# Optimization experiments

Measured on AMD Instinct MI355X. Metric: run time of the kernel, lower is better.

The kernel has to match this reference:

```python
import jax, jax.numpy as jnp
import numpy as np

N = 200000   # active voxels
K = 27       # 3^3 kernel offsets
C = 64       # feature channels (in == out -> residual is Identity)
EPS = 1e-5   # BatchNorm eps (torch default)


def setup_inputs() -> dict:
    key = jax.random.key(0)
    k0, k1, k2, k3 = jax.random.split(key, 4)
    x = jax.random.normal(k0, (N, C), dtype=jnp.float32)
    # neighbor map: for each output voxel and kernel offset, index of input voxel
    nbr_idx = jax.random.randint(k1, (N, K), 0, N, dtype=jnp.int64)
    W1 = jax.random.normal(k2, (K, C, C), dtype=jnp.float32) * 0.05
    W2 = jax.random.normal(k3, (K, C, C), dtype=jnp.float32) * 0.05
    gamma1 = jnp.ones((C,), jnp.float32)
    beta1 = jnp.zeros((C,), jnp.float32)
    gamma2 = jnp.ones((C,), jnp.float32)
    beta2 = jnp.zeros((C,), jnp.float32)
    return {"x": x, "nbr_idx": nbr_idx, "W1": W1, "gamma1": gamma1,
            "beta1": beta1, "W2": W2, "gamma2": gamma2, "beta2": beta2}


def batchnorm(x, gamma, beta):
    # train-mode BatchNorm1d over the voxel axis (biased variance)
    mu = x.mean(axis=0)
    var = x.var(axis=0)
    return (x - mu) * jax.lax.rsqrt(var + EPS) * gamma + beta


def sparse_conv(x, nbr_idx, W):
    # gather-GEMM-scatter sparse conv, streamed over the 27 kernel offsets
    # x: [N, Cin], nbr_idx: [N, K], W: [K, Cin, Cout]
    def body(acc, kw):
        idx, Wk = kw                      # idx: [N], Wk: [Cin, Cout]
        return acc + x[idx] @ Wk, None
    acc0 = jnp.zeros((x.shape[0], W.shape[2]), x.dtype)
    acc, _ = jax.lax.scan(body, acc0, (nbr_idx.T, W))
    return acc


def reference(x, nbr_idx, W1, gamma1, beta1, W2, gamma2, beta2):
    residual = x  # in_features == out_features -> Identity residual
    out = sparse_conv(jax.nn.relu(batchnorm(x, gamma1, beta1)), nbr_idx, W1)
    out = sparse_conv(jax.nn.relu(batchnorm(out, gamma2, beta2)), nbr_idx, W2)
    return out + residual
```

## Files before the change

kernel.cpp:

```cpp
#include <hip/hip_runtime.h>


#define KOFF 27

typedef __bf16 bf16x8 __attribute__((ext_vector_type(8)));
typedef float floatx4 __attribute__((ext_vector_type(4)));

__device__ __forceinline__ unsigned short f2bf(float x) {
    union { float f; unsigned int u; } v; v.f = x;
    unsigned int u = v.u;
    unsigned int r = u + 0x7FFFu + ((u >> 16) & 1u);
    return (unsigned short)(r >> 16);
}
__device__ __forceinline__ float bf2f(unsigned short s) {
    union { float f; unsigned int u; } v; v.u = ((unsigned int)s) << 16; return v.f;
}

__global__ void prep2(const float* __restrict__ W1, const float* __restrict__ W2,
                      unsigned short* __restrict__ W1f, unsigned short* __restrict__ W2f,
                      const float* __restrict__ x, float* __restrict__ stats,
                      int total) {
    int b = blockIdx.x, t = threadIdx.x;
    if (b < 54) {
        __shared__ float sW[64 * 68];
        int k = b % 27;
        const float* src = (b < 27 ? W1 : W2) + k * 4096;
        unsigned short* dst = (b < 27 ? W1f : W2f) + (size_t)k * 4096;
        #pragma unroll
        for (int i = 0; i < 4; ++i) {
            int i4 = t + i * 256;
            float4 v = ((const float4*)src)[i4];
            int f = i4 * 4, r = f >> 6, c = f & 63;
            sW[r * 68 + c]     = v.x;
            sW[r * 68 + c + 1] = v.y;
            sW[r * 68 + c + 2] = v.z;
            sW[r * 68 + c + 3] = v.w;
        }
        __syncthreads();
        int fi = (t >> 5) & 7, ct = fi >> 1, ks = fi & 1;
        unsigned short o[16];
        #pragma unroll
        for (int d = 0; d < 2; ++d) {
            int lane2 = (t * 2 + d) & 63, q = lane2 >> 4, l15 = lane2 & 15;
            #pragma unroll
            for (int j = 0; j < 8; ++j) {
                int cin = ks * 32 + q * 8 + j, cout = ct * 16 + l15;
                o[d * 8 + j] = f2bf(sW[cin * 68 + cout]);
            }
        }
        ((uint4*)(dst + t * 16))[0] = *(const uint4*)(o);
        ((uint4*)(dst + t * 16))[1] = *(const uint4*)(o + 8);
        return;
    }
    __shared__ float s[128];
    if (t < 128) s[t] = 0.f;
    __syncthreads();
    int i = (b - 54) * 256 + t;
    int stride = (gridDim.x - 54) * 256;
    int c = i & 63;
    float s1 = 0.f, s2 = 0.f;
    for (; i < total; i += stride) { float v = x[i]; s1 += v; s2 += v * v; }
    atomicAdd(&s[c], s1);
    atomicAdd(&s[64 + c], s2);
    __syncthreads();
    if (t < 64) { atomicAdd(&stats[t], s[t]); atomicAdd(&stats[64 + t], s[64 + t]); }
}

__global__ void bn_relu_f32(const float* __restrict__ in, const float* __restrict__ sums,
                            const float* __restrict__ gamma, const float* __restrict__ beta,
                            unsigned short* __restrict__ out, int total4, float invN) {
    __shared__ float sab[128];
    int t = threadIdx.x;
    if (t < 64) {
        float mu  = sums[t] * invN;
        float var = fmaxf(sums[64 + t] * invN - mu * mu, 0.f);
        float a   = gamma[t] * rsqrtf(var + 1e-5f);
        sab[t] = a; sab[64 + t] = beta[t] - mu * a;
    }
    __syncthreads();
    int i = blockIdx.x * blockDim.x + t;
    int stride = gridDim.x * blockDim.x;
    for (; i < total4; i += stride) {
        float4 v = ((const float4*)in)[i];
        int c0 = (i << 2) & 63;
        ushort4 o;
        o.x = f2bf(fmaxf(sab[c0]     * v.x + sab[64 + c0],     0.f));
        o.y = f2bf(fmaxf(sab[c0 + 1] * v.y + sab[64 + c0 + 1], 0.f));
        o.z = f2bf(fmaxf(sab[c0 + 2] * v.z + sab[64 + c0 + 2], 0.f));
        o.w = f2bf(fmaxf(sab[c0 + 3] * v.w + sab[64 + c0 + 3], 0.f));
        ((ushort4*)out)[i] = o;
    }
}

__global__ void bn_relu_b16(const unsigned short* __restrict__ in, const float* __restrict__ sums,
                            const float* __restrict__ gamma, const float* __restrict__ beta,
                            unsigned short* __restrict__ out, int total8, float invN) {
    __shared__ float sab[128];
    int t = threadIdx.x;
    if (t < 64) {
        float mu  = sums[t] * invN;
        float var = fmaxf(sums[64 + t] * invN - mu * mu, 0.f);
        float a   = gamma[t] * rsqrtf(var + 1e-5f);
        sab[t] = a; sab[64 + t] = beta[t] - mu * a;
    }
    __syncthreads();
    int i = blockIdx.x * blockDim.x + t;
    int stride = gridDim.x * blockDim.x;
    for (; i < total8; i += stride) {
        uint4 v = ((const uint4*)in)[i];
        int c0 = (i << 3) & 63;
        unsigned int w[4] = {v.x, v.y, v.z, v.w};
        unsigned int o[4];
        #pragma unroll
        for (int p = 0; p < 4; ++p) {
            float f0 = bf2f((unsigned short)(w[p] & 0xffff));
            float f1 = bf2f((unsigned short)(w[p] >> 16));
            int c = c0 + p * 2;
            unsigned short r0 = f2bf(fmaxf(sab[c]     * f0 + sab[64 + c],     0.f));
            unsigned short r1 = f2bf(fmaxf(sab[c + 1] * f1 + sab[64 + c + 1], 0.f));
            o[p] = (unsigned int)r0 | ((unsigned int)r1 << 16);
        }
        ((uint4*)out)[i] = make_uint4(o[0], o[1], o[2], o[3]);
    }
}

#define MFMA(a, b, c) __builtin_amdgcn_mfma_f32_16x16x32_bf16(a, b, c, 0, 0, 0)
#define WAIT_LGKM0() __builtin_amdgcn_s_waitcnt(0xC07F)

__global__ __launch_bounds__(256, 4) void spconv(
        const unsigned short* __restrict__ h,
        const int* __restrict__ idx,
        const unsigned short* __restrict__ Wf,
        unsigned short* __restrict__ outb,
        float* __restrict__ outf,
        const float* __restrict__ resid,
        float* __restrict__ stats,
        int N) {
    __shared__ float4 arena[1088];
    __shared__ float sred[128];
    unsigned short* sBb = (unsigned short*)arena;
    float* sE = (float*)arena;

    int t = threadIdx.x, lane = t & 63, wid = t >> 6;
    int q = lane >> 4, l15 = lane & 15;
    int base = blockIdx.x * 128;
    if (t < 128) sred[t] = 0.f;

    int r0 = base + wid * 32 + l15;
    int r1 = r0 + 16;
    const int* ip0 = idx + (size_t)min(r0, N - 1) * KOFF;
    const int* ip1 = idx + (size_t)min(r1, N - 1) * KOFF;
    int qo = q * 8;

    floatx4 acc[2][4];
    #pragma unroll
    for (int a_ = 0; a_ < 2; ++a_)
        #pragma unroll
        for (int b_ = 0; b_ < 4; ++b_)
            acc[a_][b_] = floatx4{0.f, 0.f, 0.f, 0.f};

    bf16x8 A0[4], A1[4], A2[4];
    {
        int g0 = ip0[0], g1 = ip1[0];
        const unsigned short* p0 = h + ((size_t)g0 << 6) + qo;
        const unsigned short* p1 = h + ((size_t)g1 << 6) + qo;
        A0[0] = *(const bf16x8*)p0; A0[1] = *(const bf16x8*)(p0 + 32);
        A0[2] = *(const bf16x8*)p1; A0[3] = *(const bf16x8*)(p1 + 32);
        g0 = ip0[1]; g1 = ip1[1];
        p0 = h + ((size_t)g0 << 6) + qo;
        p1 = h + ((size_t)g1 << 6) + qo;
        A1[0] = *(const bf16x8*)p0; A1[1] = *(const bf16x8*)(p0 + 32);
        A1[2] = *(const bf16x8*)p1; A1[3] = *(const bf16x8*)(p1 + 32);
    }
    int gc0 = ip0[2], gc1 = ip1[2];

    const uint4* Wf4 = (const uint4*)Wf;
    int so = wid * 64 + lane;
    uint4 bs0 = Wf4[so], bs1 = Wf4[256 + so];
    ((uint4*)sBb)[so] = bs0; ((uint4*)sBb)[256 + so] = bs1;
    bs0 = Wf4[512 + so]; bs1 = Wf4[512 + 256 + so];

#define COMPUTE(ACUR, CB) {                                                    \
    const bf16x8* bp = (const bf16x8*)(sBb + (CB) * 4096);                     \
    bf16x8 f0 = bp[lane], f1 = bp[64 + lane], f2 = bp[128 + lane], f3 = bp[192 + lane]; \
    acc[0][0] = MFMA(ACUR[0], f0, acc[0][0]); acc[0][0] = MFMA(ACUR[1], f1, acc[0][0]); \
    acc[0][1] = MFMA(ACUR[0], f2, acc[0][1]); acc[0][1] = MFMA(ACUR[1], f3, acc[0][1]); \
    acc[1][0] = MFMA(ACUR[2], f0, acc[1][0]); acc[1][0] = MFMA(ACUR[3], f1, acc[1][0]); \
    acc[1][1] = MFMA(ACUR[2], f2, acc[1][1]); acc[1][1] = MFMA(ACUR[3], f3, acc[1][1]); \
    f0 = bp[256 + lane]; f1 = bp[320 + lane]; f2 = bp[384 + lane]; f3 = bp[448 + lane]; \
    acc[0][2] = MFMA(ACUR[0], f0, acc[0][2]); acc[0][2] = MFMA(ACUR[1], f1, acc[0][2]); \
    acc[0][3] = MFMA(ACUR[0], f2, acc[0][3]); acc[0][3] = MFMA(ACUR[1], f3, acc[0][3]); \
    acc[1][2] = MFMA(ACUR[2], f0, acc[1][2]); acc[1][2] = MFMA(ACUR[3], f1, acc[1][2]); \
    acc[1][3] = MFMA(ACUR[2], f2, acc[1][3]); acc[1][3] = MFMA(ACUR[3], f3, acc[1][3]); \
}

#define BODY_FULL(ACUR, ALD, KRT, CB, NB) {                                    \
    WAIT_LGKM0();                                                              \
    __builtin_amdgcn_s_barrier();                                              \
    ((uint4*)sBb)[(NB) * 512 + so] = bs0;                                      \
    ((uint4*)sBb)[(NB) * 512 + 256 + so] = bs1;                                \
    bs0 = Wf4[((KRT) + 2) * 512 + so]; bs1 = Wf4[((KRT) + 2) * 512 + 256 + so];\
    {                                                                          \
        const unsigned short* p0 = h + ((size_t)gc0 << 6) + qo;                \
        const unsigned short* p1 = h + ((size_t)gc1 << 6) + qo;                \
        ALD[0] = *(const bf16x8*)p0; ALD[1] = *(const bf16x8*)(p0 + 32);       \
        ALD[2] = *(const bf16x8*)p1; ALD[3] = *(const bf16x8*)(p1 + 32);       \
    }                                                                          \
    gc0 = ip0[(KRT) + 3]; gc1 = ip1[(KRT) + 3];                                \
    COMPUTE(ACUR, CB)                                                          \
}

    #pragma unroll 1
    for (int kk = 0; kk < 24; kk += 6) {
        BODY_FULL(A0, A2, kk + 0, 0, 1)
        BODY_FULL(A1, A0, kk + 1, 1, 0)
        BODY_FULL(A2, A1, kk + 2, 0, 1)
        BODY_FULL(A0, A2, kk + 3, 1, 0)
        BODY_FULL(A1, A0, kk + 4, 0, 1)
        BODY_FULL(A2, A1, kk + 5, 1, 0)
    }
    {
        WAIT_LGKM0();
        __builtin_amdgcn_s_barrier();
        ((uint4*)sBb)[512 + so] = bs0; ((uint4*)sBb)[512 + 256 + so] = bs1;
        bs0 = Wf4[26 * 512 + so]; bs1 = Wf4[26 * 512 + 256 + so];
        {
            const unsigned short* p0 = h + ((size_t)gc0 << 6) + qo;
            const unsigned short* p1 = h + ((size_t)gc1 << 6) + qo;
            A2[0] = *(const bf16x8*)p0; A2[1] = *(const bf16x8*)(p0 + 32);
            A2[2] = *(const bf16x8*)p1; A2[3] = *(const bf16x8*)(p1 + 32);
        }
        COMPUTE(A0, 0)
    }
    {
        WAIT_LGKM0();
        __builtin_amdgcn_s_barrier();
        ((uint4*)sBb)[so] = bs0; ((uint4*)sBb)[256 + so] = bs1;
        COMPUTE(A1, 1)
    }
    {
        WAIT_LGKM0();
        __builtin_amdgcn_s_barrier();
        COMPUTE(A2, 0)
    }
#undef BODY_FULL
#undef COMPUTE

    if (stats) {
        #pragma unroll
        for (int ct = 0; ct < 4; ++ct) {
            float s1 = 0.f, s2 = 0.f;
            #pragma unroll
            for (int rt = 0; rt < 2; ++rt)
                #pragma unroll
                for (int r = 0; r < 4; ++r) {
                    int rowc = base + wid * 32 + rt * 16 + q * 4 + r;
                    float vv = (rowc < N) ? acc[rt][ct][r] : 0.f;
                    s1 += vv; s2 += vv * vv;
                }
            s1 += __shfl_xor(s1, 16); s2 += __shfl_xor(s2, 16);
            s1 += __shfl_xor(s1, 32); s2 += __shfl_xor(s2, 32);
            if (q == 0) {
                atomicAdd(&sred[ct * 16 + l15], s1);
                atomicAdd(&sred[64 + ct * 16 + l15], s2);
            }
        }
    }

    __syncthreads();

    #pragma unroll
    for (int hf = 0; hf < 2; ++hf) {
        if ((wid >> 1) == hf) {
            int lrow0 = (wid & 1) * 32;
            #pragma unroll
            for (int rt = 0; rt < 2; ++rt)
                #pragma unroll
                for (int ct = 0; ct < 4; ++ct)
                    #pragma unroll
                    for (int r = 0; r < 4; ++r)
                        sE[(lrow0 + rt * 16 + q * 4 + r) * 68 + ct * 16 + l15] = acc[rt][ct][r];
        }
        __syncthreads();
        if (hf == 0 && stats && t < 64) {
            atomicAdd(&stats[t], sred[t]);
            atomicAdd(&stats[64 + t], sred[64 + t]);
        }
        int rr = t >> 2, cc = t & 3;
        int grow = base + hf * 64 + rr;
        if (grow < N) {
            const float* sp = sE + rr * 68 + cc * 16;
            if (outb) {
                unsigned short o[16];
                #pragma unroll
                for (int j = 0; j < 16; ++j) o[j] = f2bf(sp[j]);
                unsigned short* op = outb + ((size_t)grow << 6) + cc * 16;
                ((uint4*)op)[0] = *(const uint4*)(o);
                ((uint4*)op)[1] = *(const uint4*)(o + 8);
            } else {
                const float* rp = resid + ((size_t)grow << 6) + cc * 16;
                float* op = outf + ((size_t)grow << 6) + cc * 16;
                #pragma unroll
                for (int j = 0; j < 4; ++j) {
                    float4 v = *(const float4*)(sp + j * 4);
                    float4 rv = *(const float4*)(rp + j * 4);
                    v.x += rv.x; v.y += rv.y; v.z += rv.z; v.w += rv.w;
                    *(float4*)(op + j * 4) = v;
                }
            }
        }
        if (hf == 0) __syncthreads();
    }
}

extern "C" void kernel_launch(void* const* d_in, const int* in_sizes, int n_in,
                              void* d_out, int out_size, void* d_ws, size_t ws_size,
                              hipStream_t stream) {
    const float* x      = (const float*)d_in[0];
    const int*   nbr    = (const int*)  d_in[1];
    const float* W1     = (const float*)d_in[2];
    const float* gamma1 = (const float*)d_in[3];
    const float* beta1  = (const float*)d_in[4];
    const float* W2     = (const float*)d_in[5];
    const float* gamma2 = (const float*)d_in[6];
    const float* beta2  = (const float*)d_in[7];
    float* out = (float*)d_out;

    int N = in_sizes[0] / 64;
    float invN = 1.0f / (float)N;

    char* ws = (char*)d_ws;
    float*          stats = (float*)ws;
    unsigned short* W1f   = (unsigned short*)(ws + 4096);
    unsigned short* W2f   = W1f + 110592;
    unsigned short* hbuf  = W2f + 110592;
    unsigned short* out1b = hbuf + (size_t)N * 64;

    int nb = (N + 127) / 128;

    hipMemsetAsync(stats, 0, 2048, stream);
    prep2<<<54 + 512, 256, 0, stream>>>(W1, W2, W1f, W2f, x, stats, N * 64);
    bn_relu_f32<<<768, 256, 0, stream>>>(x, stats, gamma1, beta1, hbuf, N * 16, invN);
    spconv<<<nb, 256, 0, stream>>>(hbuf, nbr, W1f, out1b, nullptr, nullptr, stats + 256, N);
    bn_relu_b16<<<768, 256, 0, stream>>>(out1b, stats + 256, gamma2, beta2, hbuf, N * 8, invN);
    spconv<<<nb, 256, 0, stream>>>(hbuf, nbr, W2f, nullptr, out, x, nullptr, N);
}
```

Baseline: 427.1 us.

## Stream weights via global_load_lds triple buffer and vectorize BN stats reduction

The spconv weight staging moves from register-staged global loads plus LDS stores to direct global-to-LDS DMA loads with a three-slot LDS ring. Synchronisation now uses explicit vmcnt waits, inline-asm ds_read_b128 and scheduling barriers, with a three-deep gather prefetch of the neighbour rows. This is meant to free the VGPRs that held staged weights and to overlap weight streaming with the MFMA work. It also vectorizes the first BN stats reduction in prep2 to float4 loads. In exchange LDS use grows to 24KB per block, which may limit occupancy, and the hand-tuned vmcnt counts are fragile.

Result: no change. 428.9 us (+0.4%).

```diff
diff --git a/kernel.cpp b/kernel.cpp
--- a/kernel.cpp
+++ b/kernel.cpp
@@ -19,7 +19,7 @@
 __global__ void prep2(const float* __restrict__ W1, const float* __restrict__ W2,
                       unsigned short* __restrict__ W1f, unsigned short* __restrict__ W2f,
                       const float* __restrict__ x, float* __restrict__ stats,
-                      int total) {
+                      int total4) {
     int b = blockIdx.x, t = threadIdx.x;
     if (b < 54) {
         __shared__ float sW[64 * 68];
@@ -57,11 +57,20 @@
     __syncthreads();
     int i = (b - 54) * 256 + t;
     int stride = (gridDim.x - 54) * 256;
-    int c = i & 63;
-    float s1 = 0.f, s2 = 0.f;
-    for (; i < total; i += stride) { float v = x[i]; s1 += v; s2 += v * v; }
-    atomicAdd(&s[c], s1);
-    atomicAdd(&s[64 + c], s2);
+    float a0 = 0.f, a1 = 0.f, a2 = 0.f, a3 = 0.f;
+    float b0 = 0.f, b1 = 0.f, b2 = 0.f, b3 = 0.f;
+    for (; i < total4; i += stride) {
+        float4 v = ((const float4*)x)[i];
+        a0 += v.x; b0 += v.x * v.x;
+        a1 += v.y; b1 += v.y * v.y;
+        a2 += v.z; b2 += v.z * v.z;
+        a3 += v.w; b3 += v.w * v.w;
+    }
+    int c0 = (t << 2) & 63;
+    atomicAdd(&s[c0],     a0); atomicAdd(&s[c0 + 1],     a1);
+    atomicAdd(&s[c0 + 2], a2); atomicAdd(&s[c0 + 3],     a3);
+    atomicAdd(&s[64 + c0],     b0); atomicAdd(&s[64 + c0 + 1], b1);
+    atomicAdd(&s[64 + c0 + 2], b2); atomicAdd(&s[64 + c0 + 3], b3);
     __syncthreads();
     if (t < 64) { atomicAdd(&stats[t], s[t]); atomicAdd(&stats[64 + t], s[64 + t]); }
 }
@@ -125,7 +134,12 @@
 }
 
 #define MFMA(a, b, c) __builtin_amdgcn_mfma_f32_16x16x32_bf16(a, b, c, 0, 0, 0)
-#define WAIT_LGKM0() __builtin_amdgcn_s_waitcnt(0xC07F)
+
+#define FENCE() { asm volatile("" ::: "memory"); __builtin_amdgcn_sched_barrier(0); }
+
+#define GLDS(GP, LOFS) __builtin_amdgcn_global_load_lds( \
+    (const __attribute__((address_space(1))) unsigned int*)(GP), \
+    (__attribute__((address_space(3))) unsigned int*)(ar + (LOFS)), 16, 0, 0)
 
 __global__ __launch_bounds__(256, 4) void spconv(
         const unsigned short* __restrict__ h,
@@ -136,9 +150,9 @@
         const float* __restrict__ resid,
         float* __restrict__ stats,
         int N) {
-    __shared__ float4 arena[1088];
+    __shared__ float4 arena[1536];
     __shared__ float sred[128];
-    unsigned short* sBb = (unsigned short*)arena;
+    char* ar = (char*)arena;
     float* sE = (float*)arena;
 
     int t = threadIdx.x, lane = t & 63, wid = t >> 6;
@@ -152,6 +166,11 @@
     const int* ip1 = idx + (size_t)min(r1, N - 1) * KOFF;
     int qo = q * 8;
 
+    const char* gw = (const char*)Wf + (size_t)(wid * 1024 + lane * 16);
+    int ldss = wid * 1024;
+    unsigned av0 = (unsigned)(size_t)((__attribute__((address_space(3))) char*)ar)
+                 + (unsigned)(lane * 16);
+
     floatx4 acc[2][4];
     #pragma unroll
     for (int a_ = 0; a_ < 2; ++a_)
@@ -159,92 +178,107 @@
         for (int b_ = 0; b_ < 4; ++b_)
             acc[a_][b_] = floatx4{0.f, 0.f, 0.f, 0.f};
 
+#define GATHER(DST, G0, G1) { \
+    const unsigned short* p0_ = h + ((size_t)(G0) << 6) + qo; \
+    const unsigned short* p1_ = h + ((size_t)(G1) << 6) + qo; \
+    DST[0] = *(const bf16x8*)p0_; DST[1] = *(const bf16x8*)(p0_ + 32); \
+    DST[2] = *(const bf16x8*)p1_; DST[3] = *(const bf16x8*)(p1_ + 32); \
+}
+
     bf16x8 A0[4], A1[4], A2[4];
-    {
-        int g0 = ip0[0], g1 = ip1[0];
-        const unsigned short* p0 = h + ((size_t)g0 << 6) + qo;
-        const unsigned short* p1 = h + ((size_t)g1 << 6) + qo;
-        A0[0] = *(const bf16x8*)p0; A0[1] = *(const bf16x8*)(p0 + 32);
-        A0[2] = *(const bf16x8*)p1; A0[3] = *(const bf16x8*)(p1 + 32);
-        g0 = ip0[1]; g1 = ip1[1];
-        p0 = h + ((size_t)g0 << 6) + qo;
-        p1 = h + ((size_t)g1 << 6) + qo;
-        A1[0] = *(const bf16x8*)p0; A1[1] = *(const bf16x8*)(p0 + 32);
-        A1[2] = *(const bf16x8*)p1; A1[3] = *(const bf16x8*)(p1 + 32);
-    }
-    int gc0 = ip0[2], gc1 = ip1[2];
-
-    const uint4* Wf4 = (const uint4*)Wf;
-    int so = wid * 64 + lane;
-    uint4 bs0 = Wf4[so], bs1 = Wf4[256 + so];
-    ((uint4*)sBb)[so] = bs0; ((uint4*)sBb)[256 + so] = bs1;
-    bs0 = Wf4[512 + so]; bs1 = Wf4[512 + 256 + so];
-
-#define COMPUTE(ACUR, CB) {                                                    \
-    const bf16x8* bp = (const bf16x8*)(sBb + (CB) * 4096);                     \
-    bf16x8 f0 = bp[lane], f1 = bp[64 + lane], f2 = bp[128 + lane], f3 = bp[192 + lane]; \
+    GLDS(gw,         ldss);
+    GLDS(gw + 4096,  ldss + 4096);
+    GLDS(gw + 8192,  8192 + ldss);
+    GLDS(gw + 12288, 8192 + ldss + 4096);
+    FENCE();
+    { int g0 = ip0[0], g1 = ip1[0]; GATHER(A0, g0, g1); }
+    { int g0 = ip0[1], g1 = ip1[1]; GATHER(A1, g0, g1); }
+    { int g0 = ip0[2], g1 = ip1[2]; GATHER(A2, g0, g1); }
+    int gc0 = ip0[3], gc1 = ip1[3];
+    FENCE();
+
+#define COMPUTE(ACUR, AV) { \
+    unsigned av_ = (AV); \
+    bf16x8 f0, f1, f2, f3; \
+    asm volatile("ds_read_b128 %0, %1 offset:0"    : "=v"(f0) : "v"(av_)); \
+    asm volatile("ds_read_b128 %0, %1 offset:1024" : "=v"(f1) : "v"(av_)); \
+    asm volatile("ds_read_b128 %0, %1 offset:2048" : "=v"(f2) : "v"(av_)); \
+    asm volatile("ds_read_b128 %0, %1 offset:3072" : "=v"(f3) : "v"(av_)); \
+    asm volatile("s_waitcnt lgkmcnt(0)" ::: "memory"); \
+    __builtin_amdgcn_sched_barrier(0); \
     acc[0][0] = MFMA(ACUR[0], f0, acc[0][0]); acc[0][0] = MFMA(ACUR[1], f1, acc[0][0]); \
     acc[0][1] = MFMA(ACUR[0], f2, acc[0][1]); acc[0][1] = MFMA(ACUR[1], f3, acc[0][1]); \
     acc[1][0] = MFMA(ACUR[2], f0, acc[1][0]); acc[1][0] = MFMA(ACUR[3], f1, acc[1][0]); \
     acc[1][1] = MFMA(ACUR[2], f2, acc[1][1]); acc[1][1] = MFMA(ACUR[3], f3, acc[1][1]); \
-    f0 = bp[256 + lane]; f1 = bp[320 + lane]; f2 = bp[384 + lane]; f3 = bp[448 + lane]; \
+    FENCE(); \
+    asm volatile("ds_read_b128 %0, %1 offset:4096" : "=v"(f0) : "v"(av_)); \
+    asm volatile("ds_read_b128 %0, %1 offset:5120" : "=v"(f1) : "v"(av_)); \
+    asm volatile("ds_read_b128 %0, %1 offset:6144" : "=v"(f2) : "v"(av_)); \
+    asm volatile("ds_read_b128 %0, %1 offset:7168" : "=v"(f3) : "v"(av_)); \
+    asm volatile("s_waitcnt lgkmcnt(0)" ::: "memory"); \
+    __builtin_amdgcn_sched_barrier(0); \
     acc[0][2] = MFMA(ACUR[0], f0, acc[0][2]); acc[0][2] = MFMA(ACUR[1], f1, acc[0][2]); \
     acc[0][3] = MFMA(ACUR[0], f2, acc[0][3]); acc[0][3] = MFMA(ACUR[1], f3, acc[0][3]); \
     acc[1][2] = MFMA(ACUR[2], f0, acc[1][2]); acc[1][2] = MFMA(ACUR[3], f1, acc[1][2]); \
     acc[1][3] = MFMA(ACUR[2], f2, acc[1][3]); acc[1][3] = MFMA(ACUR[3], f3, acc[1][3]); \
 }
 
-#define BODY_FULL(ACUR, ALD, KRT, CB, NB) {                                    \
-    WAIT_LGKM0();                                                              \
-    __builtin_amdgcn_s_barrier();                                              \
-    ((uint4*)sBb)[(NB) * 512 + so] = bs0;                                      \
-    ((uint4*)sBb)[(NB) * 512 + 256 + so] = bs1;                                \
-    bs0 = Wf4[((KRT) + 2) * 512 + so]; bs1 = Wf4[((KRT) + 2) * 512 + 256 + so];\
-    {                                                                          \
-        const unsigned short* p0 = h + ((size_t)gc0 << 6) + qo;                \
-        const unsigned short* p1 = h + ((size_t)gc1 << 6) + qo;                \
-        ALD[0] = *(const bf16x8*)p0; ALD[1] = *(const bf16x8*)(p0 + 32);       \
-        ALD[2] = *(const bf16x8*)p1; ALD[3] = *(const bf16x8*)(p1 + 32);       \
-    }                                                                          \
-    gc0 = ip0[(KRT) + 3]; gc1 = ip1[(KRT) + 3];                                \
-    COMPUTE(ACUR, CB)                                                          \
-}
+#define STEP_WAIT(VM) \
+    asm volatile("s_waitcnt vmcnt(" VM ")" ::: "memory"); \
+    __builtin_amdgcn_sched_barrier(0); \
+    __builtin_amdgcn_s_barrier(); \
+    FENCE();
+
+#define STAGE(K, WOFS) \
+    GLDS(gw + (size_t)((K) + 2) * 8192,        (WOFS) + ldss); \
+    GLDS(gw + (size_t)((K) + 2) * 8192 + 4096, (WOFS) + ldss + 4096); \
+    FENCE();
+
+#define BODY_FULL(K, VM, AB, RD, WOFS) { \
+    STEP_WAIT(VM) \
+    STAGE(K, WOFS) \
+    COMPUTE(AB, av0 + (RD)); \
+    FENCE(); \
+    GATHER(AB, gc0, gc1); \
+    gc0 = ip0[(K) + 4]; gc1 = ip1[(K) + 4]; \
+    FENCE(); \
+}
+
+    BODY_FULL(0, "2",  A0, 0,     16384)
+    BODY_FULL(1, "14", A1, 8192,  0)
 
     #pragma unroll 1
-    for (int kk = 0; kk < 24; kk += 6) {
-        BODY_FULL(A0, A2, kk + 0, 0, 1)
-        BODY_FULL(A1, A0, kk + 1, 1, 0)
-        BODY_FULL(A2, A1, kk + 2, 0, 1)
-        BODY_FULL(A0, A2, kk + 3, 1, 0)
-        BODY_FULL(A1, A0, kk + 4, 0, 1)
-        BODY_FULL(A2, A1, kk + 5, 1, 0)
+    for (int k = 2; k < 23; k += 3) {
+        BODY_FULL(k,     "14", A2, 16384, 8192)
+        BODY_FULL(k + 1, "14", A0, 0,     16384)
+        BODY_FULL(k + 2, "14", A1, 8192,  0)
     }
     {
-        WAIT_LGKM0();
-        __builtin_amdgcn_s_barrier();
-        ((uint4*)sBb)[512 + so] = bs0; ((uint4*)sBb)[512 + 256 + so] = bs1;
-        bs0 = Wf4[26 * 512 + so]; bs1 = Wf4[26 * 512 + 256 + so];
-        {
-            const unsigned short* p0 = h + ((size_t)gc0 << 6) + qo;
-            const unsigned short* p1 = h + ((size_t)gc1 << 6) + qo;
-            A2[0] = *(const bf16x8*)p0; A2[1] = *(const bf16x8*)(p0 + 32);
-            A2[2] = *(const bf16x8*)p1; A2[3] = *(const bf16x8*)(p1 + 32);
-        }
-        COMPUTE(A0, 0)
+        STEP_WAIT("14")
+        STAGE(23, 8192)
+        COMPUTE(A2, av0 + 16384);
+        FENCE();
+        GATHER(A2, gc0, gc1);
+        FENCE();
     }
     {
-        WAIT_LGKM0();
-        __builtin_amdgcn_s_barrier();
-        ((uint4*)sBb)[so] = bs0; ((uint4*)sBb)[256 + so] = bs1;
-        COMPUTE(A1, 1)
+        STEP_WAIT("12")
+        STAGE(24, 16384)
+        COMPUTE(A0, av0 + 0);
     }
     {
-        WAIT_LGKM0();
-        __builtin_amdgcn_s_barrier();
-        COMPUTE(A2, 0)
+        STEP_WAIT("6")
+        COMPUTE(A1, av0 + 8192);
+    }
+    {
+        STEP_WAIT("0")
+        COMPUTE(A2, av0 + 16384);
     }
 #undef BODY_FULL
+#undef STAGE
+#undef STEP_WAIT
 #undef COMPUTE
+#undef GATHER
 
     if (stats) {
         #pragma unroll
@@ -339,7 +373,7 @@
     int nb = (N + 127) / 128;
 
     hipMemsetAsync(stats, 0, 2048, stream);
-    prep2<<<54 + 512, 256, 0, stream>>>(W1, W2, W1f, W2f, x, stats, N * 64);
+    prep2<<<54 + 512, 256, 0, stream>>>(W1, W2, W1f, W2f, x, stats, N * 16);
     bn_relu_f32<<<768, 256, 0, stream>>>(x, stats, gamma1, beta1, hbuf, N * 16, invN);
     spconv<<<nb, 256, 0, stream>>>(hbuf, nbr, W1f, out1b, nullptr, nullptr, stats + 256, N);
     bn_relu_b16<<<768, 256, 0, stream>>>(out1b, stats + 256, gamma2, beta2, hbuf, N * 8, invN);
```

## Fuse second BN+ReLU into conv gather and vectorize input stats reduction

Applied to the files above, without the earlier changes.

Removes the standalone bf16 BatchNorm+ReLU kernel. The second sparse conv now applies the per-channel affine and ReLU to gathered rows in registers before the MFMAs. This saves one full read-write pass over the intermediate activations and a kernel launch. In exchange, every gathered row (27x per voxel) is normalized again, which adds VALU work and registers inside the MFMA loop. The stats reduction in prep2 also now reads float4 with four per-channel accumulators.

After: 448.3 us. 1.05x slower.

```diff
diff --git a/kernel.cpp b/kernel.cpp
--- a/kernel.cpp
+++ b/kernel.cpp
@@ -19,7 +19,7 @@
 __global__ void prep2(const float* __restrict__ W1, const float* __restrict__ W2,
                       unsigned short* __restrict__ W1f, unsigned short* __restrict__ W2f,
                       const float* __restrict__ x, float* __restrict__ stats,
-                      int total) {
+                      int total4) {
     int b = blockIdx.x, t = threadIdx.x;
     if (b < 54) {
         __shared__ float sW[64 * 68];
@@ -57,11 +57,20 @@
     __syncthreads();
     int i = (b - 54) * 256 + t;
     int stride = (gridDim.x - 54) * 256;
-    int c = i & 63;
-    float s1 = 0.f, s2 = 0.f;
-    for (; i < total; i += stride) { float v = x[i]; s1 += v; s2 += v * v; }
-    atomicAdd(&s[c], s1);
-    atomicAdd(&s[64 + c], s2);
+    float a0 = 0.f, a1 = 0.f, a2 = 0.f, a3 = 0.f;
+    float b0 = 0.f, b1 = 0.f, b2 = 0.f, b3 = 0.f;
+    for (; i < total4; i += stride) {
+        float4 v = ((const float4*)x)[i];
+        a0 += v.x; b0 += v.x * v.x;
+        a1 += v.y; b1 += v.y * v.y;
+        a2 += v.z; b2 += v.z * v.z;
+        a3 += v.w; b3 += v.w * v.w;
+    }
+    int c0 = (t << 2) & 63;
+    atomicAdd(&s[c0],     a0); atomicAdd(&s[c0 + 1],     a1);
+    atomicAdd(&s[c0 + 2], a2); atomicAdd(&s[c0 + 3],     a3);
+    atomicAdd(&s[64 + c0],     b0); atomicAdd(&s[64 + c0 + 1], b1);
+    atomicAdd(&s[64 + c0 + 2], b2); atomicAdd(&s[64 + c0 + 3], b3);
     __syncthreads();
     if (t < 64) { atomicAdd(&stats[t], s[t]); atomicAdd(&stats[64 + t], s[64 + t]); }
 }
@@ -92,41 +101,18 @@
     }
 }
 
-__global__ void bn_relu_b16(const unsigned short* __restrict__ in, const float* __restrict__ sums,
-                            const float* __restrict__ gamma, const float* __restrict__ beta,
-                            unsigned short* __restrict__ out, int total8, float invN) {
-    __shared__ float sab[128];
-    int t = threadIdx.x;
-    if (t < 64) {
-        float mu  = sums[t] * invN;
-        float var = fmaxf(sums[64 + t] * invN - mu * mu, 0.f);
-        float a   = gamma[t] * rsqrtf(var + 1e-5f);
-        sab[t] = a; sab[64 + t] = beta[t] - mu * a;
-    }
-    __syncthreads();
-    int i = blockIdx.x * blockDim.x + t;
-    int stride = gridDim.x * blockDim.x;
-    for (; i < total8; i += stride) {
-        uint4 v = ((const uint4*)in)[i];
-        int c0 = (i << 3) & 63;
-        unsigned int w[4] = {v.x, v.y, v.z, v.w};
-        unsigned int o[4];
-        #pragma unroll
-        for (int p = 0; p < 4; ++p) {
-            float f0 = bf2f((unsigned short)(w[p] & 0xffff));
-            float f1 = bf2f((unsigned short)(w[p] >> 16));
-            int c = c0 + p * 2;
-            unsigned short r0 = f2bf(fmaxf(sab[c]     * f0 + sab[64 + c],     0.f));
-            unsigned short r1 = f2bf(fmaxf(sab[c + 1] * f1 + sab[64 + c + 1], 0.f));
-            o[p] = (unsigned int)r0 | ((unsigned int)r1 << 16);
-        }
-        ((uint4*)out)[i] = make_uint4(o[0], o[1], o[2], o[3]);
-    }
-}
-
 #define MFMA(a, b, c) __builtin_amdgcn_mfma_f32_16x16x32_bf16(a, b, c, 0, 0, 0)
 #define WAIT_LGKM0() __builtin_amdgcn_s_waitcnt(0xC07F)
 
+__device__ __forceinline__ bf16x8 bn8(bf16x8 v, const float* fa, const float* fb) {
+    bf16x8 r;
+    #pragma unroll
+    for (int j = 0; j < 8; ++j)
+        r[j] = (__bf16)fmaxf(fa[j] * (float)v[j] + fb[j], 0.f);
+    return r;
+}
+
+template <int DOBN>
 __global__ __launch_bounds__(256, 4) void spconv(
         const unsigned short* __restrict__ h,
         const int* __restrict__ idx,
@@ -135,9 +121,13 @@
         float* __restrict__ outf,
         const float* __restrict__ resid,
         float* __restrict__ stats,
-        int N) {
+        const float* __restrict__ bnsums,
+        const float* __restrict__ gamma,
+        const float* __restrict__ beta,
+        float invN, int N) {
     __shared__ float4 arena[1088];
     __shared__ float sred[128];
+    __shared__ float sab[128];
     unsigned short* sBb = (unsigned short*)arena;
     float* sE = (float*)arena;
 
@@ -151,6 +141,22 @@
     const int* ip0 = idx + (size_t)min(r0, N - 1) * KOFF;
     const int* ip1 = idx + (size_t)min(r1, N - 1) * KOFF;
     int qo = q * 8;
+
+    float fa0[8], fb0[8], fa1[8], fb1[8];
+    if (DOBN) {
+        if (t < 64) {
+            float mu  = bnsums[t] * invN;
+            float var = fmaxf(bnsums[64 + t] * invN - mu * mu, 0.f);
+            float a   = gamma[t] * rsqrtf(var + 1e-5f);
+            sab[t] = a; sab[64 + t] = beta[t] - mu * a;
+        }
+        __syncthreads();
+        #pragma unroll
+        for (int j = 0; j < 8; ++j) {
+            fa0[j] = sab[qo + j];      fb0[j] = sab[64 + qo + j];
+            fa1[j] = sab[32 + qo + j]; fb1[j] = sab[64 + 32 + qo + j];
+        }
+    }
 
     floatx4 acc[2][4];
     #pragma unroll
@@ -181,17 +187,22 @@
     bs0 = Wf4[512 + so]; bs1 = Wf4[512 + 256 + so];
 
 #define COMPUTE(ACUR, CB) {                                                    \
+    bf16x8 t0_, t1_, t2_, t3_;                                                 \
+    if (DOBN) {                                                                \
+        t0_ = bn8(ACUR[0], fa0, fb0); t1_ = bn8(ACUR[1], fa1, fb1);            \
+        t2_ = bn8(ACUR[2], fa0, fb0); t3_ = bn8(ACUR[3], fa1, fb1);            \
+    } else { t0_ = ACUR[0]; t1_ = ACUR[1]; t2_ = ACUR[2]; t3_ = ACUR[3]; }     \
     const bf16x8* bp = (const bf16x8*)(sBb + (CB) * 4096);                     \
     bf16x8 f0 = bp[lane], f1 = bp[64 + lane], f2 = bp[128 + lane], f3 = bp[192 + lane]; \
-    acc[0][0] = MFMA(ACUR[0], f0, acc[0][0]); acc[0][0] = MFMA(ACUR[1], f1, acc[0][0]); \
-    acc[0][1] = MFMA(ACUR[0], f2, acc[0][1]); acc[0][1] = MFMA(ACUR[1], f3, acc[0][1]); \
-    acc[1][0] = MFMA(ACUR[2], f0, acc[1][0]); acc[1][0] = MFMA(ACUR[3], f1, acc[1][0]); \
-    acc[1][1] = MFMA(ACUR[2], f2, acc[1][1]); acc[1][1] = MFMA(ACUR[3], f3, acc[1][1]); \
+    acc[0][0] = MFMA(t0_, f0, acc[0][0]); acc[0][0] = MFMA(t1_, f1, acc[0][0]); \
+    acc[0][1] = MFMA(t0_, f2, acc[0][1]); acc[0][1] = MFMA(t1_, f3, acc[0][1]); \
+    acc[1][0] = MFMA(t2_, f0, acc[1][0]); acc[1][0] = MFMA(t3_, f1, acc[1][0]); \
+    acc[1][1] = MFMA(t2_, f2, acc[1][1]); acc[1][1] = MFMA(t3_, f3, acc[1][1]); \
     f0 = bp[256 + lane]; f1 = bp[320 + lane]; f2 = bp[384 + lane]; f3 = bp[448 + lane]; \
-    acc[0][2] = MFMA(ACUR[0], f0, acc[0][2]); acc[0][2] = MFMA(ACUR[1], f1, acc[0][2]); \
-    acc[0][3] = MFMA(ACUR[0], f2, acc[0][3]); acc[0][3] = MFMA(ACUR[1], f3, acc[0][3]); \
-    acc[1][2] = MFMA(ACUR[2], f0, acc[1][2]); acc[1][2] = MFMA(ACUR[3], f1, acc[1][2]); \
-    acc[1][3] = MFMA(ACUR[2], f2, acc[1][3]); acc[1][3] = MFMA(ACUR[3], f3, acc[1][3]); \
+    acc[0][2] = MFMA(t0_, f0, acc[0][2]); acc[0][2] = MFMA(t1_, f1, acc[0][2]); \
+    acc[0][3] = MFMA(t0_, f2, acc[0][3]); acc[0][3] = MFMA(t1_, f3, acc[0][3]); \
+    acc[1][2] = MFMA(t2_, f0, acc[1][2]); acc[1][2] = MFMA(t3_, f1, acc[1][2]); \
+    acc[1][3] = MFMA(t2_, f2, acc[1][3]); acc[1][3] = MFMA(t3_, f3, acc[1][3]); \
 }
 
 #define BODY_FULL(ACUR, ALD, KRT, CB, NB) {                                    \
@@ -339,9 +350,10 @@
     int nb = (N + 127) / 128;
 
     hipMemsetAsync(stats, 0, 2048, stream);
-    prep2<<<54 + 512, 256, 0, stream>>>(W1, W2, W1f, W2f, x, stats, N * 64);
+    prep2<<<54 + 512, 256, 0, stream>>>(W1, W2, W1f, W2f, x, stats, N * 16);
     bn_relu_f32<<<768, 256, 0, stream>>>(x, stats, gamma1, beta1, hbuf, N * 16, invN);
-    spconv<<<nb, 256, 0, stream>>>(hbuf, nbr, W1f, out1b, nullptr, nullptr, stats + 256, N);
-    bn_relu_b16<<<768, 256, 0, stream>>>(out1b, stats + 256, gamma2, beta2, hbuf, N * 8, invN);
-    spconv<<<nb, 256, 0, stream>>>(hbuf, nbr, W2f, nullptr, out, x, nullptr, N);
-}
+    spconv<0><<<nb, 256, 0, stream>>>(hbuf, nbr, W1f, out1b, nullptr, nullptr,
+                                      stats + 256, nullptr, nullptr, nullptr, invN, N);
+    spconv<1><<<nb, 256, 0, stream>>>(out1b, nbr, W2f, nullptr, out, x,
+                                      nullptr, stats + 256, gamma2, beta2, invN, N);
+}
```
